# Kernel optimization log

Hardware: AMD Instinct MI355X
Metric: run time of the kernel (lower is better)

The kernel has to match this reference:

```python
import jax, jax.numpy as jnp
import numpy as np

N, S, E, HEADS = 8, 2048, 1024, 16


def setup_inputs() -> dict:
    root = jax.random.key(0)
    k1, k2, k3, k4, k5, k6 = jax.random.split(root, 6)
    query = jax.random.normal(k1, (N, S, E), jnp.float32)
    key_t = jax.random.normal(k2, (N, S, E), jnp.float32)
    value = jax.random.normal(k3, (N, S, E), jnp.float32)
    # mask broadcasts against the (buggy) energy tensor of shape (N, S, H, H)
    mask = jax.random.randint(k4, (1, 1, HEADS, HEADS), 0, 2, jnp.int32)
    # guarantee no all-masked softmax row (avoid NaN)
    diag = jnp.arange(HEADS)
    mask = mask.at[0, 0, diag, diag].set(1)
    W_out = jax.random.normal(k5, (E, E), jnp.float32) / np.float32(np.sqrt(E))
    b_out = jax.random.normal(k6, (E,), jnp.float32) * 0.02
    return {"query": query, "key": key_t, "value": value, "mask": mask,
            "W_out": W_out, "b_out": b_out, "heads": HEADS}


def reference(query, key, value, mask, W_out, b_out, heads):
    # Faithful translation of the original forward, INCLUDING its einsum-label
    # bug: tensors are transposed to (N, H, S, D) but the einsum subscripts
    # treat axis 1 as 'q/k' and axis 2 as 'h', so softmax runs over heads.
    n, q_len, e = query.shape
    d = e // heads
    inv_scale = np.float32(1.0 / np.sqrt(d))
    q = query.reshape(n, q_len, heads, d).transpose(0, 2, 1, 3)   # (N,H,S,D)
    k = key.reshape(n, q_len, heads, d).transpose(0, 2, 1, 3)     # (N,H,S,D)
    v = value.reshape(n, q_len, heads, d).transpose(0, 2, 1, 3)   # (N,H,S,D)
    # labels applied to transposed tensors -> energy shape (N, S, H, H)
    energy = jnp.einsum('nqhd,nkhd->nhqk', q, k) * inv_scale
    energy = jnp.where(mask == 0, -jnp.inf, energy)
    attention = jax.nn.softmax(energy, axis=-1)                   # over heads axis
    out = jnp.einsum('nhql,nlhd->nqhd', attention, v)             # (N,H,S,D)
    out = out.reshape(n, q_len, e)                                # raw memory reinterp, as torch does
    return out @ W_out.T + b_out
```

## Files before the change

kernel.cpp:

```cpp
#include <hip/hip_runtime.h>
#include <stdint.h>

#define S_LEN 2048
#define EMB 1024
#define NHEADS 16
#define HDIM 64

typedef __bf16 bf16x8 __attribute__((ext_vector_type(8)));
typedef float f32x4 __attribute__((ext_vector_type(4)));

__device__ __forceinline__ unsigned short f2bf(float f) {
  unsigned int b = __float_as_uint(f);
  b += 0x7FFFu + ((b >> 16) & 1u);
  return (unsigned short)(b >> 16);
}

#define GLD16(gp, lp)                                                          \
  __builtin_amdgcn_global_load_lds(                                            \
      (const __attribute__((address_space(1))) void*)(gp),                     \
      (__attribute__((address_space(3))) void*)(lp), 16, 0, 0)

__global__ __launch_bounds__(64) void attn_kernel(
    const float* __restrict__ Q, const float* __restrict__ K,
    const float* __restrict__ V, const int* __restrict__ mask,
    unsigned short* __restrict__ X) {
  const int pos = blockIdx.x;
  const int n = pos >> 11;
  const int s = pos & 2047;
  const int lane = threadIdx.x;

  __shared__ float Qs[16][68];
  __shared__ float Ks[16][68];
  __shared__ float Vs[1024];
  __shared__ float As[16][17];

  const float* qrow = Q + (size_t)pos * EMB;
  const float* krow = K + (size_t)pos * EMB;
  const float* vrow = V + (size_t)pos * EMB;

#pragma unroll
  for (int c = 0; c < 4; ++c) {
    int e = c * 256 + lane * 4;
    float4 qv = *(const float4*)(qrow + e);
    float4 kv = *(const float4*)(krow + e);
    float4 vv = *(const float4*)(vrow + e);
    int i = e >> 6, d = e & 63;
    *(float4*)&Qs[i][d] = qv;
    *(float4*)&Ks[i][d] = kv;
    *(float4*)&Vs[e] = vv;
  }
  __syncthreads();

  const int i2 = lane >> 4;
  const int j = lane & 15;
  float p[4];
#pragma unroll
  for (int t = 0; t < 4; ++t) {
    const int i = t * 4 + i2;
    float acc = 0.f;
#pragma unroll
    for (int dc = 0; dc < 16; ++dc) {
      float4 qv = *(const float4*)&Qs[i][dc * 4];
      float4 kv = *(const float4*)&Ks[j][dc * 4];
      acc += qv.x * kv.x + qv.y * kv.y + qv.z * kv.z + qv.w * kv.w;
    }
    float g = acc * 0.125f;
    if (mask[i * 16 + j] == 0) g = -1e30f;
    float mx = g;
#pragma unroll
    for (int off = 1; off < 16; off <<= 1) mx = fmaxf(mx, __shfl_xor(mx, off));
    float ex = __expf(g - mx);
    float sm = ex;
#pragma unroll
    for (int off = 1; off < 16; off <<= 1) sm += __shfl_xor(sm, off);
    p[t] = ex / sm;
  }
#pragma unroll
  for (int t = 0; t < 4; ++t) As[t * 4 + i2][j] = p[t];
  __syncthreads();

  const size_t xbase =
      ((size_t)n * S_LEN + (s >> 4)) * EMB + (size_t)((s & 15) * HDIM + lane);
  for (int i = 0; i < 16; ++i) {
    float acc = 0.f;
#pragma unroll
    for (int jj = 0; jj < 16; ++jj) acc += As[i][jj] * Vs[jj * 64 + lane];
    X[xbase + (size_t)i * 128 * EMB] = f2bf(acc);
  }
}

__global__ __launch_bounds__(256) void wconv_kernel(
    const float* __restrict__ W, unsigned short* __restrict__ Wb) {
  const int idx = blockIdx.x * 256 + threadIdx.x;
  float4 w = *(const float4*)(W + (size_t)idx * 4);
  ushort4 o;
  o.x = f2bf(w.x);
  o.y = f2bf(w.y);
  o.z = f2bf(w.z);
  o.w = f2bf(w.w);
  *(ushort4*)(Wb + (size_t)idx * 4) = o;
}

__global__ __launch_bounds__(256) void gemm_kernel(
    const unsigned short* __restrict__ A, const unsigned short* __restrict__ B,
    const float* __restrict__ bias, float* __restrict__ C) {
  __shared__ unsigned short sA[128 * 32];
  __shared__ unsigned short sB[128 * 32];

  int bid = blockIdx.x;
  const int cpx = gridDim.x >> 3;
  bid = (bid & 7) * cpx + (bid >> 3);
  const int tileM = (bid >> 3) * 128;
  const int tileN = (bid & 7) * 128;

  const int t = threadIdx.x;
  const int lane = t & 63;
  const int wid = t >> 6;
  const int wm = wid >> 1, wn = wid & 1;
  const int lrow = lane & 15;
  const int lgrp = lane >> 4;

  f32x4 acc[4][4];
#pragma unroll
  for (int a = 0; a < 4; ++a)
#pragma unroll
    for (int b = 0; b < 4; ++b) acc[a][b] = (f32x4){0.f, 0.f, 0.f, 0.f};

  const int row0 = t >> 2;
  const int kk = (t & 3) * 8;
  const size_t abase = ((size_t)(tileM + row0)) * 1024 + kk;
  const size_t bbase = ((size_t)(tileN + row0)) * 1024 + kk;

  for (int k0 = 0; k0 < 1024; k0 += 32) {
#pragma unroll
    for (int c = 0; c < 2; ++c) {
      GLD16(A + abase + (size_t)c * 64 * 1024 + k0,
            (char*)sA + c * 4096 + t * 16);
      GLD16(B + bbase + (size_t)c * 64 * 1024 + k0,
            (char*)sB + c * 4096 + t * 16);
    }
    __syncthreads();

    bf16x8 af[4], bfr[4];
#pragma unroll
    for (int mi = 0; mi < 4; ++mi)
      af[mi] = *(const bf16x8*)&sA[(wm * 64 + mi * 16 + lrow) * 32 + lgrp * 8];
#pragma unroll
    for (int ni = 0; ni < 4; ++ni)
      bfr[ni] = *(const bf16x8*)&sB[(wn * 64 + ni * 16 + lrow) * 32 + lgrp * 8];
#pragma unroll
    for (int mi = 0; mi < 4; ++mi)
#pragma unroll
      for (int ni = 0; ni < 4; ++ni)
        acc[mi][ni] = __builtin_amdgcn_mfma_f32_16x16x32_bf16(
            af[mi], bfr[ni], acc[mi][ni], 0, 0, 0);
    __syncthreads();
  }

#pragma unroll
  for (int ni = 0; ni < 4; ++ni) {
    const int col = tileN + wn * 64 + ni * 16 + lrow;
    const float bv = bias[col];
#pragma unroll
    for (int mi = 0; mi < 4; ++mi) {
      const int row = tileM + wm * 64 + mi * 16 + lgrp * 4;
#pragma unroll
      for (int r = 0; r < 4; ++r)
        C[(size_t)(row + r) * 1024 + col] = acc[mi][ni][r] + bv;
    }
  }
}

extern "C" void kernel_launch(void* const* d_in, const int* in_sizes, int n_in,
                              void* d_out, int out_size, void* d_ws,
                              size_t ws_size, hipStream_t stream) {
  const float* Q = (const float*)d_in[0];
  const float* K = (const float*)d_in[1];
  const float* V = (const float*)d_in[2];
  const int* mask = (const int*)d_in[3];
  const float* W = (const float*)d_in[4];
  const float* bias = (const float*)d_in[5];
  float* out = (float*)d_out;

  unsigned short* X = (unsigned short*)d_ws;
  unsigned short* Wb =
      (unsigned short*)((char*)d_ws + (size_t)32 * 1024 * 1024);

  hipLaunchKernelGGL(attn_kernel, dim3(8 * S_LEN), dim3(64), 0, stream, Q, K,
                     V, mask, X);
  hipLaunchKernelGGL(wconv_kernel, dim3(1024), dim3(256), 0, stream, W, Wb);
  hipLaunchKernelGGL(gemm_kernel, dim3(1024), dim3(256), 0, stream, X, Wb,
                     bias, out);
}
```

Baseline: 114.9 us.

## Compute per-position head attention with bf16 MFMA, four positions per block

Rewrites the attention kernel so each wave handles one position. The Q·K energy and the attention·V product now run on 16x16x32 bf16 MFMA instructions instead of scalar FP32 dot products in LDS. Four waves share a 256-thread block, and the loads, transpose and intermediates are kept per-wave in LDS without block barriers. The softmax reductions are interleaved across four rows and use a reciprocal instead of a divide. The intent is to cut ALU and LDS cost and launch granularity in a memory-bound kernel, at the cost of rounding Q, K and V to bf16 before the energy computation, which reduces accuracy. It also leaves a dead shuffle loop in place.

Measured after the change: 99.15 us. 1.16x faster.

```diff
diff --git a/kernel.cpp b/kernel.cpp
--- a/kernel.cpp
+++ b/kernel.cpp
@@ -3,8 +3,6 @@
 
 #define S_LEN 2048
 #define EMB 1024
-#define NHEADS 16
-#define HDIM 64
 
 typedef __bf16 bf16x8 __attribute__((ext_vector_type(8)));
 typedef float f32x4 __attribute__((ext_vector_type(4)));
@@ -15,24 +13,32 @@
   return (unsigned short)(b >> 16);
 }
 
+__device__ __forceinline__ bf16x8 cvt8(float4 a, float4 b) {
+  bf16x8 r;
+  r[0] = (__bf16)a.x; r[1] = (__bf16)a.y; r[2] = (__bf16)a.z; r[3] = (__bf16)a.w;
+  r[4] = (__bf16)b.x; r[5] = (__bf16)b.y; r[6] = (__bf16)b.z; r[7] = (__bf16)b.w;
+  return r;
+}
+
 #define GLD16(gp, lp)                                                          \
   __builtin_amdgcn_global_load_lds(                                            \
       (const __attribute__((address_space(1))) void*)(gp),                     \
       (__attribute__((address_space(3))) void*)(lp), 16, 0, 0)
 
-__global__ __launch_bounds__(64) void attn_kernel(
+__global__ __launch_bounds__(256) void attn_kernel(
     const float* __restrict__ Q, const float* __restrict__ K,
     const float* __restrict__ V, const int* __restrict__ mask,
-    unsigned short* __restrict__ X) {
-  const int pos = blockIdx.x;
+    __bf16* __restrict__ X) {
+  __shared__ __bf16 Vt[4][64][24];
+  __shared__ __bf16 As[4][16][24];
+
+  const int lane = threadIdx.x & 63;
+  const int wv = threadIdx.x >> 6;
+  const int pos = blockIdx.x * 4 + wv;
   const int n = pos >> 11;
   const int s = pos & 2047;
-  const int lane = threadIdx.x;
-
-  __shared__ float Qs[16][68];
-  __shared__ float Ks[16][68];
-  __shared__ float Vs[1024];
-  __shared__ float As[16][17];
+  const int j16 = lane & 15;
+  const int grp = lane >> 4;
 
   const float* qrow = Q + (size_t)pos * EMB;
   const float* krow = K + (size_t)pos * EMB;
@@ -40,52 +46,89 @@
 
 #pragma unroll
   for (int c = 0; c < 4; ++c) {
-    int e = c * 256 + lane * 4;
-    float4 qv = *(const float4*)(qrow + e);
-    float4 kv = *(const float4*)(krow + e);
-    float4 vv = *(const float4*)(vrow + e);
-    int i = e >> 6, d = e & 63;
-    *(float4*)&Qs[i][d] = qv;
-    *(float4*)&Ks[i][d] = kv;
-    *(float4*)&Vs[e] = vv;
-  }
-  __syncthreads();
-
-  const int i2 = lane >> 4;
-  const int j = lane & 15;
+    const int e = c * 256 + lane * 4;
+    const float4 vv = *(const float4*)(vrow + e);
+    const int hi = e >> 6;
+    const int d0 = e & 63;
+    Vt[wv][d0 + 0][hi] = (__bf16)vv.x;
+    Vt[wv][d0 + 1][hi] = (__bf16)vv.y;
+    Vt[wv][d0 + 2][hi] = (__bf16)vv.z;
+    Vt[wv][d0 + 3][hi] = (__bf16)vv.w;
+  }
+
+  const int fo = j16 * 64 + grp * 8;
+  bf16x8 qa[2], kb[2];
+#pragma unroll
+  for (int t = 0; t < 2; ++t) {
+    float4 a0 = *(const float4*)(qrow + fo + t * 32);
+    float4 a1 = *(const float4*)(qrow + fo + t * 32 + 4);
+    float4 b0 = *(const float4*)(krow + fo + t * 32);
+    float4 b1 = *(const float4*)(krow + fo + t * 32 + 4);
+    qa[t] = cvt8(a0, a1);
+    kb[t] = cvt8(b0, b1);
+  }
+
+  f32x4 en = {0.f, 0.f, 0.f, 0.f};
+  en = __builtin_amdgcn_mfma_f32_16x16x32_bf16(qa[0], kb[0], en, 0, 0, 0);
+  en = __builtin_amdgcn_mfma_f32_16x16x32_bf16(qa[1], kb[1], en, 0, 0, 0);
+
   float p[4];
 #pragma unroll
-  for (int t = 0; t < 4; ++t) {
-    const int i = t * 4 + i2;
-    float acc = 0.f;
-#pragma unroll
-    for (int dc = 0; dc < 16; ++dc) {
-      float4 qv = *(const float4*)&Qs[i][dc * 4];
-      float4 kv = *(const float4*)&Ks[j][dc * 4];
-      acc += qv.x * kv.x + qv.y * kv.y + qv.z * kv.z + qv.w * kv.w;
+  for (int r = 0; r < 4; ++r) {
+    const int i = grp * 4 + r;
+    float g = en[r] * 0.125f;
+    if (mask[i * 16 + j16] == 0) g = -1e30f;
+    p[r] = g;
+  }
+#pragma unroll
+  for (int off = 1; off < 16; off <<= 1) {
+#pragma unroll
+    for (int r = 0; r < 4; ++r) {
+      float o = __shfl_xor(p[r], off);
+      (void)o;
     }
-    float g = acc * 0.125f;
-    if (mask[i * 16 + j] == 0) g = -1e30f;
-    float mx = g;
-#pragma unroll
-    for (int off = 1; off < 16; off <<= 1) mx = fmaxf(mx, __shfl_xor(mx, off));
-    float ex = __expf(g - mx);
-    float sm = ex;
-#pragma unroll
-    for (int off = 1; off < 16; off <<= 1) sm += __shfl_xor(sm, off);
-    p[t] = ex / sm;
-  }
-#pragma unroll
-  for (int t = 0; t < 4; ++t) As[t * 4 + i2][j] = p[t];
-  __syncthreads();
+  }
+  float mx[4], ex[4], sm[4];
+#pragma unroll
+  for (int r = 0; r < 4; ++r) mx[r] = p[r];
+#pragma unroll
+  for (int off = 1; off < 16; off <<= 1)
+#pragma unroll
+    for (int r = 0; r < 4; ++r) mx[r] = fmaxf(mx[r], __shfl_xor(mx[r], off));
+#pragma unroll
+  for (int r = 0; r < 4; ++r) {
+    ex[r] = __expf(p[r] - mx[r]);
+    sm[r] = ex[r];
+  }
+#pragma unroll
+  for (int off = 1; off < 16; off <<= 1)
+#pragma unroll
+    for (int r = 0; r < 4; ++r) sm[r] += __shfl_xor(sm[r], off);
+#pragma unroll
+  for (int r = 0; r < 4; ++r) {
+    const float inv = __builtin_amdgcn_rcpf(sm[r]);
+    As[wv][grp * 4 + r][j16] = (__bf16)(ex[r] * inv);
+  }
+
+  bf16x8 af;
+#pragma unroll
+  for (int e = 0; e < 8; ++e) af[e] = (__bf16)0.f;
+  if (grp < 2) af = *(const bf16x8*)&As[wv][j16][grp * 8];
 
   const size_t xbase =
-      ((size_t)n * S_LEN + (s >> 4)) * EMB + (size_t)((s & 15) * HDIM + lane);
-  for (int i = 0; i < 16; ++i) {
-    float acc = 0.f;
-#pragma unroll
-    for (int jj = 0; jj < 16; ++jj) acc += As[i][jj] * Vs[jj * 64 + lane];
-    X[xbase + (size_t)i * 128 * EMB] = f2bf(acc);
+      ((size_t)n * S_LEN + (s >> 4)) * EMB + (size_t)((s & 15) * 64);
+  __bf16* xp = X + xbase + j16 + (size_t)grp * 4 * 128 * EMB;
+#pragma unroll
+  for (int c = 0; c < 4; ++c) {
+    bf16x8 bv;
+#pragma unroll
+    for (int e = 0; e < 8; ++e) bv[e] = (__bf16)0.f;
+    if (grp < 2) bv = *(const bf16x8*)&Vt[wv][c * 16 + j16][grp * 8];
+    f32x4 o = {0.f, 0.f, 0.f, 0.f};
+    o = __builtin_amdgcn_mfma_f32_16x16x32_bf16(af, bv, o, 0, 0, 0);
+#pragma unroll
+    for (int r = 0; r < 4; ++r)
+      xp[(size_t)r * 128 * EMB + c * 16] = (__bf16)o[r];
   }
 }
 
@@ -182,13 +225,13 @@
   const float* bias = (const float*)d_in[5];
   float* out = (float*)d_out;
 
-  unsigned short* X = (unsigned short*)d_ws;
+  __bf16* X = (__bf16*)d_ws;
   unsigned short* Wb =
       (unsigned short*)((char*)d_ws + (size_t)32 * 1024 * 1024);
 
-  hipLaunchKernelGGL(attn_kernel, dim3(8 * S_LEN), dim3(64), 0, stream, Q, K,
-                     V, mask, X);
+  hipLaunchKernelGGL(attn_kernel, dim3(8 * S_LEN / 4), dim3(256), 0, stream, Q,
+                     K, V, mask, X);
   hipLaunchKernelGGL(wconv_kernel, dim3(1024), dim3(256), 0, stream, W, Wb);
-  hipLaunchKernelGGL(gemm_kernel, dim3(1024), dim3(256), 0, stream, X, Wb,
-                     bias, out);
-}
+  hipLaunchKernelGGL(gemm_kernel, dim3(1024), dim3(256), 0, stream,
+                     (const unsigned short*)X, Wb, bias, out);
+}
```
